# Kernel tuning notes

Measured on AMD Instinct MI355X. Metric: run time of the kernel, lower is better.

Reference implementation:

```python
import jax, jax.numpy as jnp
import numpy as np

B, T, F, OS, OF, NC = 128, 2048, 512, 20, 42, 10  # batch, time, feat, output_size, out_features, classes
BN_EPS = 1e-5


def setup_inputs() -> dict:
    key = jax.random.key(0)
    ks = jax.random.split(key, 10)
    y = jax.random.normal(ks[0], (B, T, F), jnp.float32)
    lengths = jax.random.randint(ks[1], (B,), T // 2, T + 1)
    lengths = lengths.at[0].set(T)  # max(lengths) must equal T so pooled time == OS

    def w(k, shape):
        return (jax.random.normal(k, shape, jnp.float32) * 0.02)

    return dict(
        y=y,
        lengths=lengths,
        bn_gamma=jnp.ones((F,), jnp.float32),
        bn_beta=jnp.zeros((F,), jnp.float32),
        W1=w(ks[2], (OF, F)), b1=jnp.zeros((OF,), jnp.float32),
        W2=w(ks[3], (OF, OF)), b2=jnp.zeros((OF,), jnp.float32),
        W3=w(ks[4], (OF, 2 * OF)), b3=jnp.zeros((OF,), jnp.float32),
        W4=w(ks[5], (OF, 3 * OF)), b4=jnp.zeros((OF,), jnp.float32),
        W5=w(ks[6], (OF, 4 * OF)), b5=jnp.zeros((OF,), jnp.float32),
        Wlin=w(ks[7], (NC, 5 * OF * OS)), blin=jnp.zeros((NC,), jnp.float32),
    )


def _varlen_mean_pool(y, lengths):
    # out[b,t,f] = mean_{s in [t, t+fs_b)} y[b,s,f], fs_b = lengths_b - OS + 1
    # (equivalent to the torch grouped-conv2d with per-sample box filters)
    fs = (lengths - OS + 1).astype(jnp.int32)  # [B]
    cs = jnp.concatenate(
        [jnp.zeros((y.shape[0], 1, y.shape[2]), y.dtype), jnp.cumsum(y, axis=1)], axis=1
    )  # [B, T+1, F]
    end_idx = fs[:, None] + jnp.arange(OS, dtype=jnp.int32)[None, :]  # [B, OS]
    ends = jnp.take_along_axis(cs, end_idx[:, :, None], axis=1)  # [B, OS, F]
    starts = cs[:, :OS, :]
    return (ends - starts) / fs.astype(y.dtype)[:, None, None]


def reference(y, lengths, bn_gamma, bn_beta, W1, b1, W2, b2, W3, b3, W4, b4, W5, b5, Wlin, blin):
    relu = jax.nn.relu
    x = _varlen_mean_pool(y, lengths)          # [B, OS, F]
    x = jnp.transpose(x, (0, 2, 1))            # [B, F, OS]
    # BatchNorm1d (training-mode batch stats, biased variance, as in torch default)
    mu = jnp.mean(x, axis=(0, 2), keepdims=True)
    var = jnp.var(x, axis=(0, 2), keepdims=True)
    x = (x - mu) * jax.lax.rsqrt(var + BN_EPS)
    x = x * bn_gamma[None, :, None] + bn_beta[None, :, None]

    def pconv(W, b, z):  # 1x1 conv1d == pointwise channel mix
        return jnp.einsum('oc,bcl->bol', W, z) + b[None, :, None]

    c1 = relu(pconv(W1, b1, x))
    c2 = relu(pconv(W2, b2, c1))
    d2 = relu(jnp.concatenate([c1, c2], axis=1))
    c3 = relu(pconv(W3, b3, d2))
    d3 = relu(jnp.concatenate([c1, c2, c3], axis=1))
    c4 = relu(pconv(W4, b4, d3))
    d4 = relu(jnp.concatenate([c1, c2, c3, c4], axis=1))
    c5 = relu(pconv(W5, b5, d4))
    d5 = relu(jnp.concatenate([c1, c2, c3, c4, c5], axis=1))  # [B, 5*OF, OS]
    flat = d5.reshape(d5.shape[0], -1)  # [B, 4200]
    logits = flat @ Wlin.T + blin
    return jax.nn.softmax(logits, axis=1)
```

## Files before the change

### kernel.cpp

```cpp
#include <hip/hip_runtime.h>
#include <math.h>

namespace {

constexpr int B  = 128;
constexpr int T  = 2048;
constexpr int F  = 512;
constexpr int OS = 20;
constexpr int OF = 42;
constexpr int NC = 10;
constexpr int NCHUNK  = 32;
constexpr int CHUNK_T = T / NCHUNK;
constexpr float BN_EPS = 1e-5f;

__global__ __launch_bounds__(256) void pool_partial_kernel(
    const float4* __restrict__ y4, const int* __restrict__ lengths,
    float4* __restrict__ mpart)
{
    const int chunk = blockIdx.x;
    const int b     = blockIdx.y;
    const int tid   = threadIdx.x;
    const int f4    = tid & 127;
    const int trow  = tid >> 7;
    const int fs    = lengths[b] - (OS - 1);
    const int t0    = chunk * CHUNK_T;

    const float4* __restrict__ base = y4 + (size_t)b * T * (F / 4) + f4;
    float4 acc = make_float4(0.f, 0.f, 0.f, 0.f);

    #pragma unroll 8
    for (int i = 0; i < CHUNK_T / 2; ++i) {
        const int t = t0 + 2 * i + trow;
        if (t >= OS - 1 && t < fs) {
            const float4 v = base[(size_t)t * (F / 4)];
            acc.x += v.x; acc.y += v.y; acc.z += v.z; acc.w += v.w;
        }
    }

    __shared__ float4 smem[F / 4];
    if (trow == 1) smem[f4] = acc;
    __syncthreads();
    if (trow == 0) {
        const float4 o = smem[f4];
        acc.x += o.x; acc.y += o.y; acc.z += o.z; acc.w += o.w;
        mpart[((size_t)b * NCHUNK + chunk) * (F / 4) + f4] = acc;
    }
}

__global__ __launch_bounds__(512) void pool_finish_kernel(
    const float* __restrict__ y, const int* __restrict__ lengths,
    const float* __restrict__ mpart, float* __restrict__ xpt,
    float* __restrict__ bnsum, float* __restrict__ bnsq)
{
    const int b  = blockIdx.x;
    const int f  = threadIdx.x;
    const int fs = lengths[b] - (OS - 1);

    float M = 0.f;
    #pragma unroll
    for (int c = 0; c < NCHUNK; ++c)
        M += mpart[((size_t)b * NCHUNK + c) * F + f];

    const float* __restrict__ yb = y + (size_t)b * T * F + f;
    float head[OS - 1], tail[OS - 1];
    #pragma unroll
    for (int j = 0; j < OS - 1; ++j) head[j] = yb[(size_t)j * F];
    #pragma unroll
    for (int j = 0; j < OS - 1; ++j) tail[j] = yb[(size_t)(fs + j) * F];

    float hs = 0.f;
    #pragma unroll
    for (int j = 0; j < OS - 1; ++j) hs += head[j];
    float tp = 0.f;

    const float inv = 1.f / (float)fs;
    float bs = 0.f, bq = 0.f;
    float* __restrict__ xo = xpt + ((size_t)b * F + f) * OS;

    #pragma unroll
    for (int s = 0; s < OS; ++s) {
        if (s > 0) { hs -= head[s - 1]; tp += tail[s - 1]; }
        const float x = (M + hs + tp) * inv;
        xo[s] = x;
        bs += x; bq += x * x;
    }
    bnsum[b * F + f] = bs;
    bnsq[b * F + f]  = bq;
}

__global__ __launch_bounds__(64) void bn_stats_kernel(
    const float* __restrict__ bnsum, const float* __restrict__ bnsq,
    const float* __restrict__ gamma, const float* __restrict__ beta,
    float* __restrict__ scale, float* __restrict__ shift)
{
    const int f = blockIdx.x * 64 + threadIdx.x;
    float s = 0.f, q = 0.f;
    for (int b = 0; b < B; ++b) {
        s += bnsum[b * F + f];
        q += bnsq[b * F + f];
    }
    const float n    = (float)(B * OS);
    const float mu   = s / n;
    const float var  = q / n - mu * mu;
    const float rstd = rsqrtf(var + BN_EPS);
    const float sc   = rstd * gamma[f];
    scale[f] = sc;
    shift[f] = beta[f] - mu * sc;
}

__device__ __forceinline__ void pconv_layer(
    int tid, int Cin, const float* __restrict__ W, const float* __restrict__ bias,
    const float* __restrict__ src, float* __restrict__ dst)
{
    if (tid < OF * 5) {
        const int o  = tid / 5;
        const int l0 = (tid % 5) * 4;
        const float bv = bias[o];
        float4 acc = make_float4(bv, bv, bv, bv);
        const float* __restrict__ wrow = W + (size_t)o * Cin;
        for (int f = 0; f < Cin; ++f) {
            const float4 xv = *reinterpret_cast<const float4*>(src + f * OS + l0);
            const float  w  = wrow[f];
            acc.x = fmaf(w, xv.x, acc.x);
            acc.y = fmaf(w, xv.y, acc.y);
            acc.z = fmaf(w, xv.z, acc.z);
            acc.w = fmaf(w, xv.w, acc.w);
        }
        acc.x = fmaxf(acc.x, 0.f); acc.y = fmaxf(acc.y, 0.f);
        acc.z = fmaxf(acc.z, 0.f); acc.w = fmaxf(acc.w, 0.f);
        *reinterpret_cast<float4*>(dst + o * OS + l0) = acc;
    }
}

__global__ __launch_bounds__(256) void mlp_kernel(
    const float* __restrict__ xpt,
    const float* __restrict__ scale, const float* __restrict__ shift,
    const float* __restrict__ W1, const float* __restrict__ b1,
    const float* __restrict__ W2, const float* __restrict__ b2,
    const float* __restrict__ W3, const float* __restrict__ b3,
    const float* __restrict__ W4, const float* __restrict__ b4,
    const float* __restrict__ W5, const float* __restrict__ b5,
    const float* __restrict__ Wlin, const float* __restrict__ blin,
    float* __restrict__ out)
{
    const int b   = blockIdx.x;
    const int tid = threadIdx.x;
    __shared__ float xs[F * OS];
    __shared__ float dd[5 * OF * OS];
    __shared__ float red[4];
    __shared__ float lg[NC];

    const float* __restrict__ xin = xpt + (size_t)b * F * OS;
    for (int i = tid; i < F * OS; i += 256) {
        const int f = i / OS;
        xs[i] = fmaf(xin[i], scale[f], shift[f]);
    }
    __syncthreads();

    pconv_layer(tid, F,      W1, b1, xs, dd);              __syncthreads();
    pconv_layer(tid, OF,     W2, b2, dd, dd + 1 * OF * OS); __syncthreads();
    pconv_layer(tid, 2 * OF, W3, b3, dd, dd + 2 * OF * OS); __syncthreads();
    pconv_layer(tid, 3 * OF, W4, b4, dd, dd + 3 * OF * OS); __syncthreads();
    pconv_layer(tid, 4 * OF, W5, b5, dd, dd + 4 * OF * OS); __syncthreads();

    float pk[NC];
    #pragma unroll
    for (int k = 0; k < NC; ++k) pk[k] = 0.f;
    for (int j = tid; j < 5 * OF * OS / 4; j += 256) {
        const float4 v = *reinterpret_cast<const float4*>(dd + j * 4);
        #pragma unroll
        for (int k = 0; k < NC; ++k) {
            const float4 w = *reinterpret_cast<const float4*>(
                Wlin + (size_t)k * (5 * OF * OS) + j * 4);
            pk[k] += v.x * w.x + v.y * w.y + v.z * w.z + v.w * w.w;
        }
    }
    #pragma unroll
    for (int k = 0; k < NC; ++k) {
        float p = pk[k];
        #pragma unroll
        for (int off = 32; off > 0; off >>= 1) p += __shfl_down(p, off);
        if ((tid & 63) == 0) red[tid >> 6] = p;
        __syncthreads();
        if (tid == 0) lg[k] = red[0] + red[1] + red[2] + red[3] + blin[k];
        __syncthreads();
    }

    if (tid == 0) {
        float m = lg[0];
        #pragma unroll
        for (int k = 1; k < NC; ++k) m = fmaxf(m, lg[k]);
        float e[NC]; float s = 0.f;
        #pragma unroll
        for (int k = 0; k < NC; ++k) { e[k] = expf(lg[k] - m); s += e[k]; }
        const float is = 1.f / s;
        #pragma unroll
        for (int k = 0; k < NC; ++k) out[b * NC + k] = e[k] * is;
    }
}

}

extern "C" void kernel_launch(void* const* d_in, const int* in_sizes, int n_in,
                              void* d_out, int out_size, void* d_ws, size_t ws_size,
                              hipStream_t stream)
{
    const float* y       = (const float*)d_in[0];
    const int*   lengths = (const int*)d_in[1];
    const float* gamma   = (const float*)d_in[2];
    const float* beta    = (const float*)d_in[3];
    const float* W1      = (const float*)d_in[4];
    const float* b1      = (const float*)d_in[5];
    const float* W2      = (const float*)d_in[6];
    const float* b2      = (const float*)d_in[7];
    const float* W3      = (const float*)d_in[8];
    const float* b3      = (const float*)d_in[9];
    const float* W4      = (const float*)d_in[10];
    const float* b4      = (const float*)d_in[11];
    const float* W5      = (const float*)d_in[12];
    const float* b5      = (const float*)d_in[13];
    const float* Wlin    = (const float*)d_in[14];
    const float* blin    = (const float*)d_in[15];
    float* out = (float*)d_out;

    float* ws    = (float*)d_ws;
    float* mpart = ws;
    float* xpt   = mpart + (size_t)B * NCHUNK * F;
    float* bnsum = xpt + (size_t)B * F * OS;
    float* bnsq  = bnsum + (size_t)B * F;
    float* scale = bnsq + (size_t)B * F;
    float* shift = scale + F;

    pool_partial_kernel<<<dim3(NCHUNK, B), 256, 0, stream>>>(
        (const float4*)y, lengths, (float4*)mpart);
    pool_finish_kernel<<<dim3(B), 512, 0, stream>>>(
        y, lengths, mpart, xpt, bnsum, bnsq);
    bn_stats_kernel<<<dim3(F / 64), 64, 0, stream>>>(
        bnsum, bnsq, gamma, beta, scale, shift);
    mlp_kernel<<<dim3(B), 256, 0, stream>>>(
        xpt, scale, shift, W1, b1, W2, b2, W3, b3, W4, b4, W5, b5,
        Wlin, blin, out);
}
```

Measured before the change: 136.9 us.

## Fuse BN stats into MLP kernel, tighten pool loop bounds, use nontemporal loads

Removes the separate bn_stats kernel launch by having every MLP block recompute the BatchNorm scale/shift from the per-batch partial sums and keep them in shared memory. The pooling loop now runs only over the clamped valid time range instead of testing each step, uses nontemporal vector loads, and accumulates with native vector adds. The logit reduction now needs one barrier pair instead of one per class. In exchange, all 128 MLP blocks redundantly read the 2x128x512 BN partial sums.

```diff
diff --git a/kernel.cpp b/kernel.cpp
--- a/kernel.cpp
+++ b/kernel.cpp
@@ -13,9 +13,11 @@
 constexpr int CHUNK_T = T / NCHUNK;
 constexpr float BN_EPS = 1e-5f;
 
+typedef float vfloat4 __attribute__((ext_vector_type(4)));
+
 __global__ __launch_bounds__(256) void pool_partial_kernel(
-    const float4* __restrict__ y4, const int* __restrict__ lengths,
-    float4* __restrict__ mpart)
+    const vfloat4* __restrict__ y4, const int* __restrict__ lengths,
+    vfloat4* __restrict__ mpart)
 {
     const int chunk = blockIdx.x;
     const int b     = blockIdx.y;
@@ -24,25 +26,23 @@
     const int trow  = tid >> 7;
     const int fs    = lengths[b] - (OS - 1);
     const int t0    = chunk * CHUNK_T;
-
-    const float4* __restrict__ base = y4 + (size_t)b * T * (F / 4) + f4;
-    float4 acc = make_float4(0.f, 0.f, 0.f, 0.f);
-
-    #pragma unroll 8
-    for (int i = 0; i < CHUNK_T / 2; ++i) {
-        const int t = t0 + 2 * i + trow;
-        if (t >= OS - 1 && t < fs) {
-            const float4 v = base[(size_t)t * (F / 4)];
-            acc.x += v.x; acc.y += v.y; acc.z += v.z; acc.w += v.w;
-        }
-    }
-
-    __shared__ float4 smem[F / 4];
+    const int lo    = (t0 > OS - 1) ? t0 : OS - 1;
+    const int hi    = (t0 + CHUNK_T < fs) ? t0 + CHUNK_T : fs;
+
+    const vfloat4* __restrict__ base = y4 + (size_t)b * T * (F / 4) + f4;
+    vfloat4 acc = {0.f, 0.f, 0.f, 0.f};
+
+    #pragma unroll 4
+    for (int t = lo + trow; t < hi; t += 2) {
+        const vfloat4 v = __builtin_nontemporal_load(&base[(size_t)t * (F / 4)]);
+        acc += v;
+    }
+
+    __shared__ vfloat4 smem[F / 4];
     if (trow == 1) smem[f4] = acc;
     __syncthreads();
     if (trow == 0) {
-        const float4 o = smem[f4];
-        acc.x += o.x; acc.y += o.y; acc.z += o.z; acc.w += o.w;
+        acc += smem[f4];
         mpart[((size_t)b * NCHUNK + chunk) * (F / 4) + f4] = acc;
     }
 }
@@ -86,26 +86,6 @@
     }
     bnsum[b * F + f] = bs;
     bnsq[b * F + f]  = bq;
-}
-
-__global__ __launch_bounds__(64) void bn_stats_kernel(
-    const float* __restrict__ bnsum, const float* __restrict__ bnsq,
-    const float* __restrict__ gamma, const float* __restrict__ beta,
-    float* __restrict__ scale, float* __restrict__ shift)
-{
-    const int f = blockIdx.x * 64 + threadIdx.x;
-    float s = 0.f, q = 0.f;
-    for (int b = 0; b < B; ++b) {
-        s += bnsum[b * F + f];
-        q += bnsq[b * F + f];
-    }
-    const float n    = (float)(B * OS);
-    const float mu   = s / n;
-    const float var  = q / n - mu * mu;
-    const float rstd = rsqrtf(var + BN_EPS);
-    const float sc   = rstd * gamma[f];
-    scale[f] = sc;
-    shift[f] = beta[f] - mu * sc;
 }
 
 __device__ __forceinline__ void pconv_layer(
@@ -134,7 +114,8 @@
 
 __global__ __launch_bounds__(256) void mlp_kernel(
     const float* __restrict__ xpt,
-    const float* __restrict__ scale, const float* __restrict__ shift,
+    const float* __restrict__ bnsum, const float* __restrict__ bnsq,
+    const float* __restrict__ gamma, const float* __restrict__ beta,
     const float* __restrict__ W1, const float* __restrict__ b1,
     const float* __restrict__ W2, const float* __restrict__ b2,
     const float* __restrict__ W3, const float* __restrict__ b3,
@@ -147,17 +128,35 @@
     const int tid = threadIdx.x;
     __shared__ float xs[F * OS];
     __shared__ float dd[5 * OF * OS];
-    __shared__ float red[4];
-    __shared__ float lg[NC];
+    __shared__ float sscale[F];
+    __shared__ float sshift[F];
+    __shared__ float red[NC][4];
+    __shared__ float lgs[NC];
+
+    for (int f = tid; f < F; f += 256) {
+        float s = 0.f, q = 0.f;
+        #pragma unroll 8
+        for (int bb = 0; bb < B; ++bb) {
+            s += bnsum[bb * F + f];
+            q += bnsq[bb * F + f];
+        }
+        const float n    = (float)(B * OS);
+        const float mu   = s / n;
+        const float var  = q / n - mu * mu;
+        const float sc   = rsqrtf(var + BN_EPS) * gamma[f];
+        sscale[f] = sc;
+        sshift[f] = beta[f] - mu * sc;
+    }
+    __syncthreads();
 
     const float* __restrict__ xin = xpt + (size_t)b * F * OS;
     for (int i = tid; i < F * OS; i += 256) {
         const int f = i / OS;
-        xs[i] = fmaf(xin[i], scale[f], shift[f]);
-    }
-    __syncthreads();
-
-    pconv_layer(tid, F,      W1, b1, xs, dd);              __syncthreads();
+        xs[i] = fmaf(xin[i], sscale[f], sshift[f]);
+    }
+    __syncthreads();
+
+    pconv_layer(tid, F,      W1, b1, xs, dd);               __syncthreads();
     pconv_layer(tid, OF,     W2, b2, dd, dd + 1 * OF * OS); __syncthreads();
     pconv_layer(tid, 2 * OF, W3, b3, dd, dd + 2 * OF * OS); __syncthreads();
     pconv_layer(tid, 3 * OF, W4, b4, dd, dd + 3 * OF * OS); __syncthreads();
@@ -175,24 +174,27 @@
             pk[k] += v.x * w.x + v.y * w.y + v.z * w.z + v.w * w.w;
         }
     }
+    const int lane = tid & 63;
+    const int wid  = tid >> 6;
     #pragma unroll
     for (int k = 0; k < NC; ++k) {
         float p = pk[k];
         #pragma unroll
         for (int off = 32; off > 0; off >>= 1) p += __shfl_down(p, off);
-        if ((tid & 63) == 0) red[tid >> 6] = p;
-        __syncthreads();
-        if (tid == 0) lg[k] = red[0] + red[1] + red[2] + red[3] + blin[k];
-        __syncthreads();
-    }
+        if (lane == 0) red[k][wid] = p;
+    }
+    __syncthreads();
+    if (tid < NC)
+        lgs[tid] = red[tid][0] + red[tid][1] + red[tid][2] + red[tid][3] + blin[tid];
+    __syncthreads();
 
     if (tid == 0) {
-        float m = lg[0];
-        #pragma unroll
-        for (int k = 1; k < NC; ++k) m = fmaxf(m, lg[k]);
+        float m = lgs[0];
+        #pragma unroll
+        for (int k = 1; k < NC; ++k) m = fmaxf(m, lgs[k]);
         float e[NC]; float s = 0.f;
         #pragma unroll
-        for (int k = 0; k < NC; ++k) { e[k] = expf(lg[k] - m); s += e[k]; }
+        for (int k = 0; k < NC; ++k) { e[k] = expf(lgs[k] - m); s += e[k]; }
         const float is = 1.f / s;
         #pragma unroll
         for (int k = 0; k < NC; ++k) out[b * NC + k] = e[k] * is;
@@ -228,16 +230,12 @@
     float* xpt   = mpart + (size_t)B * NCHUNK * F;
     float* bnsum = xpt + (size_t)B * F * OS;
     float* bnsq  = bnsum + (size_t)B * F;
-    float* scale = bnsq + (size_t)B * F;
-    float* shift = scale + F;
 
     pool_partial_kernel<<<dim3(NCHUNK, B), 256, 0, stream>>>(
-        (const float4*)y, lengths, (float4*)mpart);
+        (const vfloat4*)y, lengths, (vfloat4*)mpart);
     pool_finish_kernel<<<dim3(B), 512, 0, stream>>>(
         y, lengths, mpart, xpt, bnsum, bnsq);
-    bn_stats_kernel<<<dim3(F / 64), 64, 0, stream>>>(
-        bnsum, bnsq, gamma, beta, scale, shift);
     mlp_kernel<<<dim3(B), 256, 0, stream>>>(
-        xpt, scale, shift, W1, b1, W2, b2, W3, b3, W4, b4, W5, b5,
+        xpt, bnsum, bnsq, gamma, beta, W1, b1, W2, b2, W3, b3, W4, b4, W5, b5,
         Wlin, blin, out);
 }
```

After: 118.0 us. 1.16x faster.
